# Optimization experiments

Hardware: AMD Instinct MI355X
Metric: run time of the kernel (lower is better)

The kernel has to match this reference:

```python
import jax, jax.numpy as jnp
import numpy as np

EMBED = 1024
BATCH = 512
K_STEPS = 96


def setup_inputs() -> dict:
    key = jax.random.key(0)
    ks = jax.random.split(key, 5)
    s = 1.0 / np.sqrt(EMBED)  # PyTorch GRU init scale
    return {
        "c": jax.random.normal(ks[0], (BATCH, EMBED), dtype=jnp.float32),
        "K": K_STEPS,
        "W_ih": jax.random.uniform(ks[1], (3 * EMBED, EMBED), minval=-s, maxval=s, dtype=jnp.float32),
        "W_hh": jax.random.uniform(ks[2], (3 * EMBED, EMBED), minval=-s, maxval=s, dtype=jnp.float32),
        "b_ih": jax.random.uniform(ks[3], (3 * EMBED,), minval=-s, maxval=s, dtype=jnp.float32),
        "b_hh": jax.random.uniform(ks[4], (3 * EMBED,), minval=-s, maxval=s, dtype=jnp.float32),
    }


def _gru_step(x, h, W_ih, W_hh, b_ih, b_hh):
    # PyTorch GRU gate order: reset, update, new
    gi = x @ W_ih.T + b_ih  # [B, 3H]
    gh = h @ W_hh.T + b_hh  # [B, 3H]
    i_r, i_z, i_n = jnp.split(gi, 3, axis=-1)
    h_r, h_z, h_n = jnp.split(gh, 3, axis=-1)
    r = jax.nn.sigmoid(i_r + h_r)
    z = jax.nn.sigmoid(i_z + h_z)
    n = jnp.tanh(i_n + r * h_n)
    return (1.0 - z) * n + z * h  # new hidden == output (seq_len=1)


def reference(c, K, W_ih, W_hh, b_ih, b_hh):
    B = c.shape[0]
    x0 = jnp.zeros((B, EMBED), dtype=c.dtype)

    def step(carry, _):
        x, h = carry
        h_new = _gru_step(x, h, W_ih, W_hh, b_ih, b_hh)
        # output y_k == h_new is fed back as next input x_{k+1}
        return (h_new, h_new), h_new

    _, ys = jax.lax.scan(step, (x0, c), None, length=K)  # ys: [K, B, H]
    return jnp.transpose(ys, (1, 0, 2))  # [B, K, H]
```

## Files before the change

kernel.cpp:

```cpp
#include <hip/hip_runtime.h>
#include <math.h>

#define H 1024
#define BATCH 512
#define KSTEPS 96
#define KH ((long)KSTEPS * H)

typedef __attribute__((ext_vector_type(8))) short short8;
typedef __attribute__((ext_vector_type(16))) float f32x16;

__device__ __forceinline__ unsigned short f2bf(float x) {
    union { float f; unsigned int u; } v; v.f = x;
    unsigned int r = v.u + 0x7fffu + ((v.u >> 16) & 1u);
    return (unsigned short)(r >> 16);
}

__device__ __forceinline__ float fsig(float x)  { return 1.f / (1.f + __expf(-x)); }
__device__ __forceinline__ float ftanh(float x) { return 1.f - 2.f / (1.f + __expf(2.f * x)); }

#define MEMFENCE asm volatile("" ::: "memory")


__global__ void prep_w(const float* __restrict__ wih,
                       const float* __restrict__ whh,
                       unsigned short* __restrict__ blob0,
                       unsigned short* __restrict__ blob1)
{
    const unsigned int f = blockIdx.x * 256 + threadIdx.x;
    const int e  = f & 7;
    const int l  = (f >> 3) & 63;
    const int kg = (f >> 9) & 1;
    const int js = (f >> 10) & 3;
    const int Jt = (f >> 12) & 31;
    const int tc = (f >> 17) & 31;
    const int b  = blockIdx.y;

    const int J = Jt * 128 + js * 32 + (l & 31);
    const int g = J & 3;
    const long j = J >> 2;
    const long k = (long)tc * 32 + kg * 16 + (l >> 5) * 8 + e;

    float v = 0.f;
    if (b == 1) {
        if (g == 0)      v = wih[j*1024 + k]           + whh[j*1024 + k];
        else if (g == 1) v = wih[(1024+j)*1024 + k]    + whh[(1024+j)*1024 + k];
        else if (g == 2) v = wih[(2048+j)*1024 + k];
        else             v = whh[(2048+j)*1024 + k];
    } else {
        if (g == 0)      v = whh[j*1024 + k];
        else if (g == 1) v = whh[(1024+j)*1024 + k];
        else if (g == 2) v = 0.f;
        else             v = whh[(2048+j)*1024 + k];
    }
    unsigned short* blob = (b == 0) ? blob0 : blob1;
    blob[f] = f2bf(v);
}

__global__ void prep_bcJ(const float* __restrict__ bih,
                         const float* __restrict__ bhh,
                         float* __restrict__ bcJ,
                         unsigned int* __restrict__ bar)
{
    const int J = blockIdx.x * 256 + threadIdx.x;
    const int g = J & 3;
    const int j = J >> 2;
    float v;
    if (g == 0)      v = bih[j]        + bhh[j];
    else if (g == 1) v = bih[1024 + j] + bhh[1024 + j];
    else if (g == 2) v = bih[2048 + j];
    else             v = bhh[2048 + j];
    bcJ[J] = v;
    if (blockIdx.x == 0) {
        bar[threadIdx.x]       = 0u;
        bar[256 + threadIdx.x] = 0u;
    }
}

__global__ void prep_h0(const float* __restrict__ cin,
                        unsigned short* __restrict__ hT)
{
    const unsigned int f = blockIdx.x * 256 + threadIdx.x;
    const int e  = f & 7;
    const int l  = (f >> 3) & 63;
    const int kg = (f >> 9) & 1;
    const int mh = (f >> 10) & 1;
    const int cc = (f >> 11) & 15;
    const int ph = (f >> 15) & 1;
    const int mt = (f >> 16) & 7;

    const long m = mt * 64 + mh * 32 + (l & 31);
    const long k = (long)(ph * 16 + cc) * 32 + kg * 16 + (l >> 5) * 8 + e;

    hT[f] = f2bf(cin[m * 1024 + k]);
}

__global__ __launch_bounds__(512) void gru_all(
    const unsigned short* __restrict__ blob0,
    const unsigned short* __restrict__ blob1,
    unsigned short* __restrict__ hTa,
    unsigned short* __restrict__ hTb,
    const float* __restrict__ cin,
    const float* __restrict__ bcJ,
    float* __restrict__ out,
    unsigned int* bar)
{
    __shared__ __attribute__((aligned(16))) char smem[65536 + 8*4608];

    const int tid  = threadIdx.x;
    const int lane = tid & 63;
    const int wv   = tid >> 6;
    const int mh   = wv & 1;
    const int js   = wv >> 1;

    const int id   = blockIdx.x;
    const int grp  = id & 7;
    const int slot = id >> 3;
    const int Jt   = grp * 4 + (slot & 3);
    const int mt   = slot >> 2;

    const float bias = bcJ[Jt * 128 + js * 32 + (lane & 31)];

    const int jj   = lane & 7;
    const long jgl = (long)Jt * 32 + js * 8 + jj;
    float hp[4];
    #pragma unroll
    for (int q = 0; q < 4; ++q) {
        const long mg = (long)mt * 64 + mh * 32 + q * 8 + (lane >> 3);
        hp[q] = cin[mg * 1024 + jgl];
    }

    char* ldsA = smem;
    float* Dw  = (float*)(smem + 65536 + wv * 4608);

    #pragma unroll 1
    for (int k = 0; k < KSTEPS; ++k) {
        const unsigned short* blob = (k == 0) ? blob0 : blob1;
        const char* wbase = (const char*)blob + (long)(Jt * 8 + js * 2) * 1024;
        const unsigned short* hTr = (k & 1) ? hTb : hTa;
        unsigned short*       hTw = (k & 1) ? hTa : hTb;
        const char* hbase = (const char*)hTr + (long)mt * 131072;
        float* outk = out + (long)k * H;

        short8 W0[2], W1[2], W2[2];

        auto loadW = [&](int c, short8* Wd) {
            const char* p = wbase + (long)c * 262144;
            asm volatile("global_load_dwordx4 %0, %1, off"
                         : "=v"(Wd[0]) : "v"(p + lane * 16) : "memory");
            asm volatile("global_load_dwordx4 %0, %1, off"
                         : "=v"(Wd[1]) : "v"(p + 1024 + lane * 16) : "memory");
        };
        auto stageA = [&](int ph) {
            const char* src = hbase + ph * 65536;
            short8 t0, t1, t2, t3, t4, t5, t6, t7;
            asm volatile("global_load_dwordx4 %0, %1, off sc0 sc1" : "=v"(t0) : "v"(src + (0*512 + tid)*16) : "memory");
            asm volatile("global_load_dwordx4 %0, %1, off sc0 sc1" : "=v"(t1) : "v"(src + (1*512 + tid)*16) : "memory");
            asm volatile("global_load_dwordx4 %0, %1, off sc0 sc1" : "=v"(t2) : "v"(src + (2*512 + tid)*16) : "memory");
            asm volatile("global_load_dwordx4 %0, %1, off sc0 sc1" : "=v"(t3) : "v"(src + (3*512 + tid)*16) : "memory");
            asm volatile("global_load_dwordx4 %0, %1, off sc0 sc1" : "=v"(t4) : "v"(src + (4*512 + tid)*16) : "memory");
            asm volatile("global_load_dwordx4 %0, %1, off sc0 sc1" : "=v"(t5) : "v"(src + (5*512 + tid)*16) : "memory");
            asm volatile("global_load_dwordx4 %0, %1, off sc0 sc1" : "=v"(t6) : "v"(src + (6*512 + tid)*16) : "memory");
            asm volatile("global_load_dwordx4 %0, %1, off sc0 sc1" : "=v"(t7) : "v"(src + (7*512 + tid)*16) : "memory");
            asm volatile("s_waitcnt vmcnt(0)" ::: "memory");
            __builtin_amdgcn_sched_barrier(0);
            *(short8*)(ldsA + (0*512 + tid)*16) = t0;
            *(short8*)(ldsA + (1*512 + tid)*16) = t1;
            *(short8*)(ldsA + (2*512 + tid)*16) = t2;
            *(short8*)(ldsA + (3*512 + tid)*16) = t3;
            *(short8*)(ldsA + (4*512 + tid)*16) = t4;
            *(short8*)(ldsA + (5*512 + tid)*16) = t5;
            *(short8*)(ldsA + (6*512 + tid)*16) = t6;
            *(short8*)(ldsA + (7*512 + tid)*16) = t7;
        };

        f32x16 acc0, acc1;
        #pragma unroll
        for (int r = 0; r < 16; ++r) { acc0[r] = bias; acc1[r] = 0.f; }

        loadW(0, W0); loadW(1, W1); loadW(2, W2);
        MEMFENCE;

        if (k > 0) {
            if (wv == 0 && lane < 32) {
                unsigned int* fp = bar + (mt * 32 + lane);
                while (true) {
                    unsigned v;
                    asm volatile("global_load_dword %0, %1, off sc0 sc1\n\t"
                                 "s_waitcnt vmcnt(0)"
                                 : "=v"(v) : "v"(fp) : "memory");
                    if (v >= (unsigned)k) break;
                    __builtin_amdgcn_s_sleep(2);
                }
            }
        }
        __syncthreads();

        stageA(0);
        __syncthreads();

        #define CHUNK(c, N, Wc, Wn)                                            \
        {                                                                      \
            asm volatile("s_waitcnt vmcnt(" #N ")" ::: "memory");              \
            __builtin_amdgcn_sched_barrier(0);                                 \
            const int cc_ = (c) & 15;                                          \
            const short8 a0_ = *(const short8*)(ldsA + ((cc_*2 + mh)*2 + 0)*1024 + lane*16); \
            const short8 a1_ = *(const short8*)(ldsA + ((cc_*2 + mh)*2 + 1)*1024 + lane*16); \
            acc0 = __builtin_amdgcn_mfma_f32_32x32x16_bf16(a0_, Wc[0], acc0, 0, 0, 0); \
            acc1 = __builtin_amdgcn_mfma_f32_32x32x16_bf16(a1_, Wc[1], acc1, 0, 0, 0); \
            if ((c) + 3 < 32) loadW((c) + 3, Wn);                              \
        }

        CHUNK(0,4,W0,W0)  CHUNK(1,4,W1,W1)  CHUNK(2,4,W2,W2)  CHUNK(3,4,W0,W0)
        CHUNK(4,4,W1,W1)  CHUNK(5,4,W2,W2)  CHUNK(6,4,W0,W0)  CHUNK(7,4,W1,W1)
        CHUNK(8,4,W2,W2)  CHUNK(9,4,W0,W0)  CHUNK(10,4,W1,W1) CHUNK(11,4,W2,W2)
        CHUNK(12,4,W0,W0) CHUNK(13,4,W1,W1) CHUNK(14,4,W2,W2) CHUNK(15,4,W0,W0)

        __syncthreads();
        stageA(1);
        __syncthreads();

        CHUNK(16,4,W1,W1) CHUNK(17,4,W2,W2) CHUNK(18,4,W0,W0) CHUNK(19,4,W1,W1)
        CHUNK(20,4,W2,W2) CHUNK(21,4,W0,W0) CHUNK(22,4,W1,W1) CHUNK(23,4,W2,W2)
        CHUNK(24,4,W0,W0) CHUNK(25,4,W1,W1) CHUNK(26,4,W2,W2) CHUNK(27,4,W0,W0)
        CHUNK(28,4,W1,W1) CHUNK(29,4,W2,W2) CHUNK(30,2,W0,W0) CHUNK(31,0,W1,W1)
        #undef CHUNK

        #pragma unroll
        for (int r = 0; r < 16; ++r) {
            const int r32 = (r & 3) + 8 * (r >> 2) + 4 * (lane >> 5);
            Dw[r32 * 36 + (lane & 31)] = acc0[r] + acc1[r];
        }
        asm volatile("s_waitcnt lgkmcnt(0)" ::: "memory");
        __builtin_amdgcn_sched_barrier(0);

        #pragma unroll
        for (int q = 0; q < 4; ++q) {
            const int m_loc = q * 8 + (lane >> 3);
            const float4 gv = *(const float4*)(Dw + m_loc * 36 + jj * 4);
            const float rr = fsig(gv.x);
            const float zz = fsig(gv.y);
            const float nn = ftanh(fmaf(rr, gv.w, gv.z));
            const float o  = nn + zz * (hp[q] - nn);
            hp[q] = o;

            const unsigned short hi = f2bf(o);
            const int j   = (int)jgl;
            const int c2  = j >> 5;
            const int kg2 = (j >> 4) & 1;
            const int lhi = (j >> 3) & 1;
            const int e2  = j & 7;
            const int ph2 = c2 >> 4;
            const int cc2 = c2 & 15;
            const int l2  = lhi * 32 + m_loc;
            const long ub = (((((long)mt*2 + ph2)*16 + cc2)*2 + mh)*2 + kg2)*512
                          + l2*8 + e2;
            unsigned short* p0 = hTw + ub;
            asm volatile("global_store_short %0, %1, off sc0 sc1"
                         :: "v"(p0), "v"((unsigned)hi) : "memory");
        }
        asm volatile("s_waitcnt vmcnt(0)" ::: "memory");
        __syncthreads();

        if (k < KSTEPS - 1 && tid == 0) {
            const unsigned kk = (unsigned)(k + 1);
            unsigned int* fp = bar + (mt * 32 + Jt);
            asm volatile("global_store_dword %0, %1, off sc0 sc1"
                         :: "v"(fp), "v"(kk) : "memory");
        }
        #pragma unroll
        for (int q = 0; q < 4; ++q) {
            const long mg = (long)mt * 64 + mh * 32 + q * 8 + (lane >> 3);
            __builtin_nontemporal_store(hp[q], &outk[mg * KH + jgl]);
        }
    }
}

extern "C" void kernel_launch(void* const* d_in, const int* in_sizes, int n_in,
                              void* d_out, int out_size, void* d_ws, size_t ws_size,
                              hipStream_t stream)
{
    const float* c   = (const float*)d_in[0];
    const float* wih = (const float*)d_in[2];
    const float* whh = (const float*)d_in[3];
    const float* bih = (const float*)d_in[4];
    const float* bhh = (const float*)d_in[5];
    float* out = (float*)d_out;

    unsigned short* blob0 = (unsigned short*)d_ws;
    unsigned short* blob1 = blob0 + 4194304L;
    float*          bcJ   = (float*)(blob1 + 4194304L);
    unsigned short* hTa   = (unsigned short*)(bcJ + 4096);
    unsigned short* hTb   = hTa + 524288L;
    unsigned int*   bar   = (unsigned int*)(hTb + 524288L);

    prep_w  <<<dim3(16384, 2), 256, 0, stream>>>(wih, whh, blob0, blob1);
    prep_bcJ<<<dim3(16),       256, 0, stream>>>(bih, bhh, bcJ, bar);
    prep_h0 <<<dim3(2048),     256, 0, stream>>>(c, hTa);

    void* args[] = { (void*)&blob0, (void*)&blob1, (void*)&hTa, (void*)&hTb,
                     (void*)&c, (void*)&bcJ, (void*)&out, (void*)&bar };
    hipLaunchCooperativeKernel((const void*)gru_all, dim3(256), dim3(512),
                               args, 0, stream);
}
```

Baseline: 834.1 us.

## Split K across wave pairs so each wave covers both M halves with one W fragment

Each wave now owns a K-half (kg) and computes both 32-row M halves, so one loaded W fragment feeds two MFMAs. This halves per-wave weight-load traffic and register use. The cost is a cross-wave reduction through a larger LDS scratch area, where two partial gate sums are added before the GRU nonlinearity. It also issues the first W loads alongside the h staging loads, and replaces some __syncthreads with raw s_barrier plus explicit waitcnts. The epilogue is reindexed so threads cover the full 64x32 tile.

```diff
diff --git a/kernel.cpp b/kernel.cpp
--- a/kernel.cpp
+++ b/kernel.cpp
@@ -104,12 +104,12 @@
     float* __restrict__ out,
     unsigned int* bar)
 {
-    __shared__ __attribute__((aligned(16))) char smem[65536 + 8*4608];
+    __shared__ __attribute__((aligned(16))) char smem[65536 + 8 * 9232];
 
     const int tid  = threadIdx.x;
     const int lane = tid & 63;
     const int wv   = tid >> 6;
-    const int mh   = wv & 1;
+    const int kg   = wv & 1;
     const int js   = wv >> 1;
 
     const int id   = blockIdx.x;
@@ -118,39 +118,38 @@
     const int Jt   = grp * 4 + (slot & 3);
     const int mt   = slot >> 2;
 
-    const float bias = bcJ[Jt * 128 + js * 32 + (lane & 31)];
-
-    const int jj   = lane & 7;
-    const long jgl = (long)Jt * 32 + js * 8 + jj;
+    const float bias = (kg == 0) ? bcJ[Jt * 128 + js * 32 + (lane & 31)] : 0.f;
+
+    char*  ldsA  = smem;
+    float* Dbase = (float*)(smem + 65536);
+    float* Dp    = Dbase + (js * 2 + kg) * 2308;
+
     float hp[4];
     #pragma unroll
     for (int q = 0; q < 4; ++q) {
-        const long mg = (long)mt * 64 + mh * 32 + q * 8 + (lane >> 3);
-        hp[q] = cin[mg * 1024 + jgl];
+        const int qi = q * 512 + tid;
+        const int jl = qi & 31;
+        const int m  = qi >> 5;
+        hp[q] = cin[((long)mt * 64 + m) * 1024 + (long)Jt * 32 + jl];
     }
-
-    char* ldsA = smem;
-    float* Dw  = (float*)(smem + 65536 + wv * 4608);
 
     #pragma unroll 1
     for (int k = 0; k < KSTEPS; ++k) {
         const unsigned short* blob = (k == 0) ? blob0 : blob1;
-        const char* wbase = (const char*)blob + (long)(Jt * 8 + js * 2) * 1024;
+        const char* wbase = (const char*)blob + (long)(Jt * 8 + js * 2 + kg) * 1024;
         const unsigned short* hTr = (k & 1) ? hTb : hTa;
         unsigned short*       hTw = (k & 1) ? hTa : hTb;
         const char* hbase = (const char*)hTr + (long)mt * 131072;
         float* outk = out + (long)k * H;
 
-        short8 W0[2], W1[2], W2[2];
-
-        auto loadW = [&](int c, short8* Wd) {
+        short8 W0, W1, W2;
+
+        auto loadW = [&](int c, short8& Wd) {
             const char* p = wbase + (long)c * 262144;
             asm volatile("global_load_dwordx4 %0, %1, off"
-                         : "=v"(Wd[0]) : "v"(p + lane * 16) : "memory");
-            asm volatile("global_load_dwordx4 %0, %1, off"
-                         : "=v"(Wd[1]) : "v"(p + 1024 + lane * 16) : "memory");
+                         : "=v"(Wd) : "v"(p + lane * 16) : "memory");
         };
-        auto stageA = [&](int ph) {
+        auto stageA = [&](int ph, bool drainAll) {
             const char* src = hbase + ph * 65536;
             short8 t0, t1, t2, t3, t4, t5, t6, t7;
             asm volatile("global_load_dwordx4 %0, %1, off sc0 sc1" : "=v"(t0) : "v"(src + (0*512 + tid)*16) : "memory");
@@ -161,7 +160,8 @@
             asm volatile("global_load_dwordx4 %0, %1, off sc0 sc1" : "=v"(t5) : "v"(src + (5*512 + tid)*16) : "memory");
             asm volatile("global_load_dwordx4 %0, %1, off sc0 sc1" : "=v"(t6) : "v"(src + (6*512 + tid)*16) : "memory");
             asm volatile("global_load_dwordx4 %0, %1, off sc0 sc1" : "=v"(t7) : "v"(src + (7*512 + tid)*16) : "memory");
-            asm volatile("s_waitcnt vmcnt(0)" ::: "memory");
+            if (drainAll) asm volatile("s_waitcnt vmcnt(0)" ::: "memory");
+            else          asm volatile("s_waitcnt vmcnt(3)" ::: "memory");
             __builtin_amdgcn_sched_barrier(0);
             *(short8*)(ldsA + (0*512 + tid)*16) = t0;
             *(short8*)(ldsA + (1*512 + tid)*16) = t1;
@@ -171,14 +171,16 @@
             *(short8*)(ldsA + (5*512 + tid)*16) = t5;
             *(short8*)(ldsA + (6*512 + tid)*16) = t6;
             *(short8*)(ldsA + (7*512 + tid)*16) = t7;
+            asm volatile("s_waitcnt lgkmcnt(0)" ::: "memory");
         };
 
-        f32x16 acc0, acc1;
+        f32x16 accLo, accHi;
         #pragma unroll
-        for (int r = 0; r < 16; ++r) { acc0[r] = bias; acc1[r] = 0.f; }
-
-        loadW(0, W0); loadW(1, W1); loadW(2, W2);
-        MEMFENCE;
+        for (int r = 0; r < 16; ++r) { accLo[r] = bias; accHi[r] = 0.f; }
+        if (kg == 0) {
+            #pragma unroll
+            for (int r = 0; r < 16; ++r) accHi[r] = bias;
+        }
 
         if (k > 0) {
             if (wv == 0 && lane < 32) {
@@ -195,71 +197,108 @@
         }
         __syncthreads();
 
-        stageA(0);
-        __syncthreads();
+        {
+            const char* src = hbase;
+        }
+        {
+            const char* src = hbase;
+            short8 t0, t1, t2, t3, t4, t5, t6, t7;
+            asm volatile("global_load_dwordx4 %0, %1, off sc0 sc1" : "=v"(t0) : "v"(src + (0*512 + tid)*16) : "memory");
+            asm volatile("global_load_dwordx4 %0, %1, off sc0 sc1" : "=v"(t1) : "v"(src + (1*512 + tid)*16) : "memory");
+            asm volatile("global_load_dwordx4 %0, %1, off sc0 sc1" : "=v"(t2) : "v"(src + (2*512 + tid)*16) : "memory");
+            asm volatile("global_load_dwordx4 %0, %1, off sc0 sc1" : "=v"(t3) : "v"(src + (3*512 + tid)*16) : "memory");
+            asm volatile("global_load_dwordx4 %0, %1, off sc0 sc1" : "=v"(t4) : "v"(src + (4*512 + tid)*16) : "memory");
+            asm volatile("global_load_dwordx4 %0, %1, off sc0 sc1" : "=v"(t5) : "v"(src + (5*512 + tid)*16) : "memory");
+            asm volatile("global_load_dwordx4 %0, %1, off sc0 sc1" : "=v"(t6) : "v"(src + (6*512 + tid)*16) : "memory");
+            asm volatile("global_load_dwordx4 %0, %1, off sc0 sc1" : "=v"(t7) : "v"(src + (7*512 + tid)*16) : "memory");
+            loadW(0, W0); loadW(1, W1); loadW(2, W2);
+            asm volatile("s_waitcnt vmcnt(3)" ::: "memory");
+            __builtin_amdgcn_sched_barrier(0);
+            *(short8*)(ldsA + (0*512 + tid)*16) = t0;
+            *(short8*)(ldsA + (1*512 + tid)*16) = t1;
+            *(short8*)(ldsA + (2*512 + tid)*16) = t2;
+            *(short8*)(ldsA + (3*512 + tid)*16) = t3;
+            *(short8*)(ldsA + (4*512 + tid)*16) = t4;
+            *(short8*)(ldsA + (5*512 + tid)*16) = t5;
+            *(short8*)(ldsA + (6*512 + tid)*16) = t6;
+            *(short8*)(ldsA + (7*512 + tid)*16) = t7;
+            asm volatile("s_waitcnt lgkmcnt(0)" ::: "memory");
+        }
+        __builtin_amdgcn_s_barrier();
 
         #define CHUNK(c, N, Wc, Wn)                                            \
         {                                                                      \
             asm volatile("s_waitcnt vmcnt(" #N ")" ::: "memory");              \
             __builtin_amdgcn_sched_barrier(0);                                 \
-            const int cc_ = (c) & 15;                                          \
-            const short8 a0_ = *(const short8*)(ldsA + ((cc_*2 + mh)*2 + 0)*1024 + lane*16); \
-            const short8 a1_ = *(const short8*)(ldsA + ((cc_*2 + mh)*2 + 1)*1024 + lane*16); \
-            acc0 = __builtin_amdgcn_mfma_f32_32x32x16_bf16(a0_, Wc[0], acc0, 0, 0, 0); \
-            acc1 = __builtin_amdgcn_mfma_f32_32x32x16_bf16(a1_, Wc[1], acc1, 0, 0, 0); \
+            const short8 aLo = *(const short8*)(ldsA + (((c)&15)*4 + kg)*1024 + lane*16);     \
+            const short8 aHi = *(const short8*)(ldsA + (((c)&15)*4 + 2 + kg)*1024 + lane*16); \
+            accLo = __builtin_amdgcn_mfma_f32_32x32x16_bf16(aLo, Wc, accLo, 0, 0, 0); \
+            accHi = __builtin_amdgcn_mfma_f32_32x32x16_bf16(aHi, Wc, accHi, 0, 0, 0); \
             if ((c) + 3 < 32) loadW((c) + 3, Wn);                              \
         }
 
-        CHUNK(0,4,W0,W0)  CHUNK(1,4,W1,W1)  CHUNK(2,4,W2,W2)  CHUNK(3,4,W0,W0)
-        CHUNK(4,4,W1,W1)  CHUNK(5,4,W2,W2)  CHUNK(6,4,W0,W0)  CHUNK(7,4,W1,W1)
-        CHUNK(8,4,W2,W2)  CHUNK(9,4,W0,W0)  CHUNK(10,4,W1,W1) CHUNK(11,4,W2,W2)
-        CHUNK(12,4,W0,W0) CHUNK(13,4,W1,W1) CHUNK(14,4,W2,W2) CHUNK(15,4,W0,W0)
-
-        __syncthreads();
-        stageA(1);
-        __syncthreads();
-
-        CHUNK(16,4,W1,W1) CHUNK(17,4,W2,W2) CHUNK(18,4,W0,W0) CHUNK(19,4,W1,W1)
-        CHUNK(20,4,W2,W2) CHUNK(21,4,W0,W0) CHUNK(22,4,W1,W1) CHUNK(23,4,W2,W2)
-        CHUNK(24,4,W0,W0) CHUNK(25,4,W1,W1) CHUNK(26,4,W2,W2) CHUNK(27,4,W0,W0)
-        CHUNK(28,4,W1,W1) CHUNK(29,4,W2,W2) CHUNK(30,2,W0,W0) CHUNK(31,0,W1,W1)
+        CHUNK(0,2,W0,W0)  CHUNK(1,2,W1,W1)  CHUNK(2,2,W2,W2)  CHUNK(3,2,W0,W0)
+        CHUNK(4,2,W1,W1)  CHUNK(5,2,W2,W2)  CHUNK(6,2,W0,W0)  CHUNK(7,2,W1,W1)
+        CHUNK(8,2,W2,W2)  CHUNK(9,2,W0,W0)  CHUNK(10,2,W1,W1) CHUNK(11,2,W2,W2)
+        CHUNK(12,2,W0,W0) CHUNK(13,2,W1,W1) CHUNK(14,2,W2,W2) CHUNK(15,2,W0,W0)
+
+        __builtin_amdgcn_s_barrier();
+        stageA(1, true);
+        __builtin_amdgcn_s_barrier();
+
+        CHUNK(16,2,W1,W1) CHUNK(17,2,W2,W2) CHUNK(18,2,W0,W0) CHUNK(19,2,W1,W1)
+        CHUNK(20,2,W2,W2) CHUNK(21,2,W0,W0) CHUNK(22,2,W1,W1) CHUNK(23,2,W2,W2)
+        CHUNK(24,2,W0,W0) CHUNK(25,2,W1,W1) CHUNK(26,2,W2,W2) CHUNK(27,2,W0,W0)
+        CHUNK(28,2,W1,W1) CHUNK(29,2,W2,W2) CHUNK(30,1,W0,W0) CHUNK(31,0,W1,W1)
         #undef CHUNK
 
         #pragma unroll
         for (int r = 0; r < 16; ++r) {
             const int r32 = (r & 3) + 8 * (r >> 2) + 4 * (lane >> 5);
-            Dw[r32 * 36 + (lane & 31)] = acc0[r] + acc1[r];
+            Dp[(r32)      * 36 + (lane & 31)] = accLo[r];
+            Dp[(32 + r32) * 36 + (lane & 31)] = accHi[r];
         }
         asm volatile("s_waitcnt lgkmcnt(0)" ::: "memory");
-        __builtin_amdgcn_sched_barrier(0);
+        __builtin_amdgcn_s_barrier();
 
         #pragma unroll
         for (int q = 0; q < 4; ++q) {
-            const int m_loc = q * 8 + (lane >> 3);
-            const float4 gv = *(const float4*)(Dw + m_loc * 36 + jj * 4);
-            const float rr = fsig(gv.x);
-            const float zz = fsig(gv.y);
-            const float nn = ftanh(fmaf(rr, gv.w, gv.z));
+            const int qi = q * 512 + tid;
+            const int jl = qi & 31;
+            const int m  = qi >> 5;
+            const int jsq = jl >> 3;
+            const int c4  = (jl & 7) * 4;
+            const float4 g0 = *(const float4*)(Dbase + (jsq*2 + 0)*2308 + m*36 + c4);
+            const float4 g1 = *(const float4*)(Dbase + (jsq*2 + 1)*2308 + m*36 + c4);
+            const float gr = g0.x + g1.x;
+            const float gz = g0.y + g1.y;
+            const float gi = g0.z + g1.z;
+            const float gh = g0.w + g1.w;
+
+            const float rr = fsig(gr);
+            const float zz = fsig(gz);
+            const float nn = ftanh(fmaf(rr, gh, gi));
             const float o  = nn + zz * (hp[q] - nn);
             hp[q] = o;
 
             const unsigned short hi = f2bf(o);
-            const int j   = (int)jgl;
+            const int j   = Jt * 32 + jl;
             const int c2  = j >> 5;
             const int kg2 = (j >> 4) & 1;
             const int lhi = (j >> 3) & 1;
             const int e2  = j & 7;
             const int ph2 = c2 >> 4;
             const int cc2 = c2 & 15;
-            const int l2  = lhi * 32 + m_loc;
-            const long ub = (((((long)mt*2 + ph2)*16 + cc2)*2 + mh)*2 + kg2)*512
+            const int mh2 = m >> 5;
+            const int l2  = lhi * 32 + (m & 31);
+            const long ub = (((((long)mt*2 + ph2)*16 + cc2)*2 + mh2)*2 + kg2)*512
                           + l2*8 + e2;
             unsigned short* p0 = hTw + ub;
             asm volatile("global_store_short %0, %1, off sc0 sc1"
                          :: "v"(p0), "v"((unsigned)hi) : "memory");
         }
         asm volatile("s_waitcnt vmcnt(0)" ::: "memory");
-        __syncthreads();
+        __builtin_amdgcn_s_barrier();
 
         if (k < KSTEPS - 1 && tid == 0) {
             const unsigned kk = (unsigned)(k + 1);
@@ -269,8 +308,11 @@
         }
         #pragma unroll
         for (int q = 0; q < 4; ++q) {
-            const long mg = (long)mt * 64 + mh * 32 + q * 8 + (lane >> 3);
-            __builtin_nontemporal_store(hp[q], &outk[mg * KH + jgl]);
+            const int qi = q * 512 + tid;
+            const int jl = qi & 31;
+            const int m  = qi >> 5;
+            __builtin_nontemporal_store(hp[q],
+                &outk[((long)mt * 64 + m) * KH + (long)Jt * 32 + jl]);
         }
     }
 }
```

New measurement: 816.3 us. 1.02x faster.
